# Performance work log

Hardware: AMD Instinct MI355X
Metric: run time of the kernel (lower is better)

The kernel has to match this reference:

```python
import jax, jax.numpy as jnp
import numpy as np

H = 128
H1 = H + 1          # 129
FUSE = H1 * H1 * H1 # 2,146,689


def setup_inputs() -> dict:
    key = jax.random.key(0)
    ks = jax.random.split(key, 9)
    B = 64
    v = jax.random.normal(ks[0], (B, H), dtype=jnp.float32)
    a = jax.random.normal(ks[1], (B, H), dtype=jnp.float32)
    t = jax.random.normal(ks[2], (B, H), dtype=jnp.float32)
    # Linear params stored as [in, out]; xavier-ish scaling
    W1 = jax.random.normal(ks[3], (FUSE, H // 2), dtype=jnp.float32) * (1.0 / np.sqrt(FUSE))
    b1 = jnp.zeros((H // 2,), dtype=jnp.float32)
    W2 = jax.random.normal(ks[4], (H // 2, H // 4), dtype=jnp.float32) * (1.0 / np.sqrt(H // 2))
    b2 = jnp.zeros((H // 4,), dtype=jnp.float32)
    W3 = jax.random.normal(ks[5], (H // 4, 1), dtype=jnp.float32) * (1.0 / np.sqrt(H // 4))
    b3 = jnp.zeros((1,), dtype=jnp.float32)
    return {"v": v, "a": a, "t": t, "W1": W1, "b1": b1,
            "W2": W2, "b2": b2, "W3": W3, "b3": b3}


def reference(v, a, t, W1, b1, W2, b2, W3, b3):
    B = a.shape[0]
    one = jnp.ones((B, 1), dtype=a.dtype)
    a_h = jnp.concatenate([one, a], axis=1)  # [B, H+1]
    v_h = jnp.concatenate([one, v], axis=1)
    t_h = jnp.concatenate([one, t], axis=1)
    # triple outer product: fusion[b,i,j,k] = a_h[b,i]*v_h[b,j]*t_h[b,k]
    fusion = jnp.einsum('bi,bj,bk->bijk', a_h, v_h, t_h).reshape(B, -1)  # [B, (H+1)^3]
    # dropout p applied at eval is identity (torch Dropout in eval / p=0)
    y1 = jax.nn.relu(fusion @ W1 + b1)
    y2 = jax.nn.relu(y1 @ W2 + b2)
    return y2 @ W3 + b3  # [B, 1]
```

## Files before the change

### kernel.cpp

```cpp
#include <hip/hip_runtime.h>
#include <hip/hip_bf16.h>

#define H 128
#define H1 129
#define NSLAB (H1 * H1)
#define KP 164
#define NBLK 1024

typedef __attribute__((ext_vector_type(8))) short short8;
typedef __attribute__((ext_vector_type(4))) float float4v;
typedef __attribute__((ext_vector_type(2))) int int2v;
typedef __attribute__((ext_vector_type(4))) int int4v;

__device__ __forceinline__ unsigned short f2bf_bits(float x) {
    return __builtin_bit_cast(unsigned short, __float2bfloat16(x));
}
__device__ __forceinline__ unsigned packbf(float x, float y) {
    return (unsigned)f2bf_bits(x) | ((unsigned)f2bf_bits(y) << 16);
}

__global__ __launch_bounds__(256, 4) void k1_partial(
        const float* __restrict__ v, const float* __restrict__ a,
        const float* __restrict__ t, const float* __restrict__ W1,
        float* __restrict__ acc)
{
    __shared__ short lds[64 * KP];

    const int tid  = threadIdx.x;
    const int wv   = tid >> 6;
    const int lane = tid & 63;
    const int quad = lane >> 4;
    const int l15  = lane & 15;

    for (int idx = tid; idx < 64 * (KP - 130); idx += 256) {
        int n = idx / (KP - 130), k = 130 + idx % (KP - 130);
        lds[n * KP + k] = 0;
    }

    short8 tf[5];
    const int bt = 16 * wv + l15;
    #pragma unroll
    for (int s = 0; s < 5; ++s) {
        #pragma unroll
        for (int j = 0; j < 8; ++j) {
            int k = 32 * s + 8 * quad + j;
            float val = (k == 0) ? 1.0f : ((k <= H) ? t[bt * H + k - 1] : 0.0f);
            tf[s][j] = (short)f2bf_bits(val);
        }
    }

    const float4v vz = {0.f, 0.f, 0.f, 0.f};
    float4v y1acc[4] = {vz, vz, vz, vz};

    const int s0 = (int)(((long long)blockIdx.x * NSLAB) / NBLK);
    const int s1 = (int)(((long long)(blockIdx.x + 1) * NSLAB) / NBLK);
    int si = s0 / H1, sj = s0 % H1;

    const int q = tid & 15;
    const int p16 = tid >> 4;

    for (int sl = s0; sl < s1; ++sl) {
        const float* Wb = W1 + (long long)sl * (H1 * 64);

        float4v ra[4], rb[4];
        #pragma unroll
        for (int it = 0; it < 4; ++it) {
            int p = it * 16 + p16;
            ra[it] = *reinterpret_cast<const float4v*>(Wb + (2 * p) * 64 + q * 4);
            rb[it] = *reinterpret_cast<const float4v*>(Wb + (2 * p + 1) * 64 + q * 4);
        }
        float lastrow = 0.f;
        if (tid < 64) lastrow = Wb[128 * 64 + tid];

        #pragma unroll
        for (int it = 0; it < 4; ++it) {
            int p = it * 16 + p16;
            #pragma unroll
            for (int c = 0; c < 4; ++c) {
                int n = q * 4 + c;
                *reinterpret_cast<unsigned*>(&lds[n * KP + 2 * p]) = packbf(ra[it][c], rb[it][c]);
            }
        }
        if (tid < 64) {
            *reinterpret_cast<unsigned*>(&lds[tid * KP + 128]) = packbf(lastrow, 0.f);
        }
        __syncthreads();

        float4v avv;
        #pragma unroll
        for (int r = 0; r < 4; ++r) {
            int br = 16 * wv + quad * 4 + r;
            float ah = (si == 0) ? 1.0f : a[br * H + si - 1];
            float vh = (sj == 0) ? 1.0f : v[br * H + sj - 1];
            avv[r] = ah * vh;
        }

        float4v D[4] = {vz, vz, vz, vz};
        #pragma unroll
        for (int s = 0; s < 5; ++s) {
            #pragma unroll
            for (int nt = 0; nt < 4; ++nt) {
                int n = nt * 16 + l15;
                int sa = n * KP + 32 * s + 8 * quad;
                int2v lo = *reinterpret_cast<const int2v*>(&lds[sa]);
                int2v hi = *reinterpret_cast<const int2v*>(&lds[sa + 4]);
                int4v w; w.x = lo.x; w.y = lo.y; w.z = hi.x; w.w = hi.y;
                short8 bf = __builtin_bit_cast(short8, w);
                D[nt] = __builtin_amdgcn_mfma_f32_16x16x32_bf16(tf[s], bf, D[nt], 0, 0, 0);
            }
        }
        #pragma unroll
        for (int nt = 0; nt < 4; ++nt) y1acc[nt] += avv * D[nt];

        __syncthreads();

        ++sj; if (sj == H1) { sj = 0; ++si; }
    }

    #pragma unroll
    for (int nt = 0; nt < 4; ++nt) {
        int h = nt * 16 + l15;
        #pragma unroll
        for (int r = 0; r < 4; ++r) {
            int br = 16 * wv + quad * 4 + r;
            unsafeAtomicAdd(&acc[br * 64 + h], y1acc[nt][r]);
        }
    }
}

__global__ void k2_tail(const float* __restrict__ acc, const float* __restrict__ b1,
                        const float* __restrict__ W2, const float* __restrict__ b2,
                        const float* __restrict__ W3, const float* __restrict__ b3,
                        float* __restrict__ out)
{
    __shared__ float y1s[64 * 64];
    __shared__ float y2s[64 * 32];
    const int tid = threadIdx.x;

    for (int e = tid; e < 64 * 64; e += 256) {
        float x = acc[e] + b1[e & 63];
        y1s[e] = x > 0.f ? x : 0.f;
    }
    __syncthreads();
    for (int e = tid; e < 64 * 32; e += 256) {
        int b = e >> 5, h2 = e & 31;
        float s = b2[h2];
        #pragma unroll 8
        for (int h = 0; h < 64; ++h) s += y1s[b * 64 + h] * W2[h * 32 + h2];
        y2s[e] = s > 0.f ? s : 0.f;
    }
    __syncthreads();
    if (tid < 64) {
        float s = b3[0];
        #pragma unroll
        for (int h2 = 0; h2 < 32; ++h2) s += y2s[tid * 32 + h2] * W3[h2];
        out[tid] = s;
    }
}

extern "C" void kernel_launch(void* const* d_in, const int* in_sizes, int n_in,
                              void* d_out, int out_size, void* d_ws, size_t ws_size,
                              hipStream_t stream) {
    const float* v  = (const float*)d_in[0];
    const float* a  = (const float*)d_in[1];
    const float* t  = (const float*)d_in[2];
    const float* W1 = (const float*)d_in[3];
    const float* b1 = (const float*)d_in[4];
    const float* W2 = (const float*)d_in[5];
    const float* b2 = (const float*)d_in[6];
    const float* W3 = (const float*)d_in[7];
    const float* b3 = (const float*)d_in[8];
    float* acc = (float*)d_ws;

    hipMemsetAsync(acc, 0, 64 * 64 * sizeof(float), stream);
    hipLaunchKernelGGL(k1_partial, dim3(NBLK), dim3(256), 0, stream, v, a, t, W1, acc);
    hipLaunchKernelGGL(k2_tail, dim3(1), dim3(256), 0, stream,
                       acc, b1, W2, b2, W3, b3, (float*)d_out);
}
```

Measured before the change: 731.7 us.

## Prefetch next W1 slab into registers during MFMA and spread atomics over replicas

The slab loop now issues global loads for the next W1 slab (and the a/v scalars) before the MFMA work on the current slab, so memory latency overlaps compute in a register double-buffer. The grid shrinks from 1024 to 768 blocks with launch bounds of 3 blocks per CU to make room for the extra prefetch registers. Atomic adds go to 8 replicated accumulators chosen by block index, which the tail kernel sums, to cut atomic contention. The cost is higher register pressure, lower occupancy, and a larger memset and reduction.

```diff
diff --git a/kernel.cpp b/kernel.cpp
--- a/kernel.cpp
+++ b/kernel.cpp
@@ -5,7 +5,8 @@
 #define H1 129
 #define NSLAB (H1 * H1)
 #define KP 164
-#define NBLK 1024
+#define NBLK 768
+#define NREP 8
 
 typedef __attribute__((ext_vector_type(8))) short short8;
 typedef __attribute__((ext_vector_type(4))) float float4v;
@@ -19,7 +20,7 @@
     return (unsigned)f2bf_bits(x) | ((unsigned)f2bf_bits(y) << 16);
 }
 
-__global__ __launch_bounds__(256, 4) void k1_partial(
+__global__ __launch_bounds__(256, 3) void k1_partial(
         const float* __restrict__ v, const float* __restrict__ a,
         const float* __restrict__ t, const float* __restrict__ W1,
         float* __restrict__ acc)
@@ -54,24 +55,28 @@
 
     const int s0 = (int)(((long long)blockIdx.x * NSLAB) / NBLK);
     const int s1 = (int)(((long long)(blockIdx.x + 1) * NSLAB) / NBLK);
-    int si = s0 / H1, sj = s0 % H1;
 
     const int q = tid & 15;
     const int p16 = tid >> 4;
-
-    for (int sl = s0; sl < s1; ++sl) {
-        const float* Wb = W1 + (long long)sl * (H1 * 64);
-
-        float4v ra[4], rb[4];
+    const int br0 = 16 * wv + quad * 4;
+
+    float4v ra[4], rb[4];
+    float lastrow;
+    float ahc[4], vhc[4], ahn[4], vhn[4];
+
+    const float* Wb = W1 + (long long)s0 * (H1 * 64);
+
+    auto ISSUE = [&](const float* Wp) {
         #pragma unroll
         for (int it = 0; it < 4; ++it) {
             int p = it * 16 + p16;
-            ra[it] = *reinterpret_cast<const float4v*>(Wb + (2 * p) * 64 + q * 4);
-            rb[it] = *reinterpret_cast<const float4v*>(Wb + (2 * p + 1) * 64 + q * 4);
-        }
-        float lastrow = 0.f;
-        if (tid < 64) lastrow = Wb[128 * 64 + tid];
-
+            ra[it] = *reinterpret_cast<const float4v*>(Wp + (2 * p) * 64 + q * 4);
+            rb[it] = *reinterpret_cast<const float4v*>(Wp + (2 * p + 1) * 64 + q * 4);
+        }
+        lastrow = (tid < 64) ? Wp[128 * 64 + tid] : 0.f;
+    };
+
+    auto WRITE = [&]() {
         #pragma unroll
         for (int it = 0; it < 4; ++it) {
             int p = it * 16 + p16;
@@ -81,20 +86,20 @@
                 *reinterpret_cast<unsigned*>(&lds[n * KP + 2 * p]) = packbf(ra[it][c], rb[it][c]);
             }
         }
-        if (tid < 64) {
+        if (tid < 64)
             *reinterpret_cast<unsigned*>(&lds[tid * KP + 128]) = packbf(lastrow, 0.f);
-        }
-        __syncthreads();
-
-        float4v avv;
+    };
+
+    auto LOADAV = [&](int si, int sj, float* ah, float* vh) {
         #pragma unroll
         for (int r = 0; r < 4; ++r) {
-            int br = 16 * wv + quad * 4 + r;
-            float ah = (si == 0) ? 1.0f : a[br * H + si - 1];
-            float vh = (sj == 0) ? 1.0f : v[br * H + sj - 1];
-            avv[r] = ah * vh;
-        }
-
+            int br = br0 + r;
+            ah[r] = (si == 0) ? 1.0f : a[br * H + si - 1];
+            vh[r] = (sj == 0) ? 1.0f : v[br * H + sj - 1];
+        }
+    };
+
+    auto MFMA_ACC = [&]() {
         float4v D[4] = {vz, vz, vz, vz};
         #pragma unroll
         for (int s = 0; s < 5; ++s) {
@@ -109,22 +114,43 @@
                 D[nt] = __builtin_amdgcn_mfma_f32_16x16x32_bf16(tf[s], bf, D[nt], 0, 0, 0);
             }
         }
+        float4v avv;
+        #pragma unroll
+        for (int r = 0; r < 4; ++r) avv[r] = ahc[r] * vhc[r];
         #pragma unroll
         for (int nt = 0; nt < 4; ++nt) y1acc[nt] += avv * D[nt];
-
+    };
+
+    int si = s0 / H1, sj = s0 % H1;
+    ISSUE(Wb);
+    LOADAV(si, sj, ahc, vhc);
+    WRITE();
+    Wb += H1 * 64;
+    int si_n = si, sj_n = sj + 1; if (sj_n == H1) { sj_n = 0; ++si_n; }
+    if (s0 + 1 < s1) { ISSUE(Wb); LOADAV(si_n, sj_n, ahn, vhn); }
+    __syncthreads();
+
+    for (int sl = s0 + 1; sl < s1; ++sl) {
+        MFMA_ACC();
+        #pragma unroll
+        for (int r = 0; r < 4; ++r) { ahc[r] = ahn[r]; vhc[r] = vhn[r]; }
         __syncthreads();
-
-        ++sj; if (sj == H1) { sj = 0; ++si; }
-    }
-
+        WRITE();
+        Wb += H1 * 64;
+        ++sj_n; if (sj_n == H1) { sj_n = 0; ++si_n; }
+        if (sl + 1 < s1) { ISSUE(Wb); LOADAV(si_n, sj_n, ahn, vhn); }
+        __syncthreads();
+    }
+    MFMA_ACC();
+
+    const int rep = blockIdx.x & (NREP - 1);
+    float* accr = acc + rep * (64 * 64);
     #pragma unroll
     for (int nt = 0; nt < 4; ++nt) {
         int h = nt * 16 + l15;
         #pragma unroll
-        for (int r = 0; r < 4; ++r) {
-            int br = 16 * wv + quad * 4 + r;
-            unsafeAtomicAdd(&acc[br * 64 + h], y1acc[nt][r]);
-        }
+        for (int r = 0; r < 4; ++r)
+            unsafeAtomicAdd(&accr[(br0 + r) * 64 + h], y1acc[nt][r]);
     }
 }
 
@@ -138,7 +164,9 @@
     const int tid = threadIdx.x;
 
     for (int e = tid; e < 64 * 64; e += 256) {
-        float x = acc[e] + b1[e & 63];
+        float x = b1[e & 63];
+        #pragma unroll
+        for (int r = 0; r < NREP; ++r) x += acc[r * 64 * 64 + e];
         y1s[e] = x > 0.f ? x : 0.f;
     }
     __syncthreads();
@@ -172,7 +200,7 @@
     const float* b3 = (const float*)d_in[8];
     float* acc = (float*)d_ws;
 
-    hipMemsetAsync(acc, 0, 64 * 64 * sizeof(float), stream);
+    hipMemsetAsync(acc, 0, NREP * 64 * 64 * sizeof(float), stream);
     hipLaunchKernelGGL(k1_partial, dim3(NBLK), dim3(256), 0, stream, v, a, t, W1, acc);
     hipLaunchKernelGGL(k2_tail, dim3(1), dim3(256), 0, stream,
                        acc, b1, W2, b2, W3, b3, (float*)d_out);
```

Result: no change. 734.7 us (+0.4%).
